# Optimization experiments

Hardware: AMD Instinct MI355X
Metric: run time of the kernel (lower is better)

Reference implementation:

```python
import math
import jax, jax.numpy as jnp
import numpy as np

D_MODEL = 1024
N_HEADS = 16
D_K = D_MODEL // N_HEADS  # 64
D_C = 256
B, S = 2, 2048


def setup_inputs() -> dict:
    key = jax.random.key(0)
    ks = jax.random.split(key, 7)
    sd = lambda fan_in: 1.0 / math.sqrt(fan_in)
    # weights stored as [in, out] so forward is x @ W
    return {
        "x": jax.random.normal(ks[0], (B, S, D_MODEL), dtype=jnp.float32),
        "W_dq": jax.random.uniform(ks[1], (D_MODEL, D_C), minval=-sd(D_MODEL), maxval=sd(D_MODEL), dtype=jnp.float32),
        "W_uq": jax.random.uniform(ks[2], (D_C, N_HEADS * D_K), minval=-sd(D_C), maxval=sd(D_C), dtype=jnp.float32),
        "W_dkv": jax.random.uniform(ks[3], (D_MODEL, D_C), minval=-sd(D_MODEL), maxval=sd(D_MODEL), dtype=jnp.float32),
        "W_uk": jax.random.uniform(ks[4], (D_C, N_HEADS * D_K), minval=-sd(D_C), maxval=sd(D_C), dtype=jnp.float32),
        "W_uv": jax.random.uniform(ks[5], (D_C, N_HEADS * D_K), minval=-sd(D_C), maxval=sd(D_C), dtype=jnp.float32),
        "W_o": jax.random.uniform(ks[6], (N_HEADS * D_K, D_MODEL), minval=-sd(N_HEADS * D_K), maxval=sd(N_HEADS * D_K), dtype=jnp.float32),
    }


def reference(x, W_dq, W_uq, W_dkv, W_uk, W_uv, W_o):
    Bx, Sx, _ = x.shape
    c_q = x @ W_dq                                   # [B,S,d_c]
    Q = (c_q @ W_uq).reshape(Bx, Sx, N_HEADS, D_K)   # [B,S,H,dk]
    c_kv = x @ W_dkv                                 # [B,S,d_c]
    K = (c_kv @ W_uk).reshape(Bx, Sx, N_HEADS, D_K)
    V = (c_kv @ W_uv).reshape(Bx, Sx, N_HEADS, D_K)
    scores = jnp.einsum("bqhd,bkhd->bhqk", Q, K) / math.sqrt(D_K)
    causal = jnp.tril(jnp.ones((Sx, Sx), dtype=bool))
    scores = jnp.where(causal, scores, -jnp.inf)
    attn = jax.nn.softmax(scores, axis=-1)           # [B,H,S,S]
    out = jnp.einsum("bhqk,bkhd->bqhd", attn, V).reshape(Bx, Sx, N_HEADS * D_K)
    return out @ W_o
```

## Files before the change

kernel.cpp:

```cpp
#include <hip/hip_runtime.h>
#include <math.h>

#define AS3 __attribute__((address_space(3)))
#define AS1 __attribute__((address_space(1)))

typedef unsigned short u16;
typedef unsigned int u32;
typedef __bf16 bf16_t;
typedef bf16_t bf16x8 __attribute__((ext_vector_type(8)));
typedef float f32x4 __attribute__((ext_vector_type(4)));
typedef float f32x16 __attribute__((ext_vector_type(16)));
typedef unsigned short u16x4 __attribute__((ext_vector_type(4)));
typedef unsigned short u16x8 __attribute__((ext_vector_type(8)));
typedef unsigned int u32x4 __attribute__((ext_vector_type(4)));

#define NH 16
#define DK 64
#define DC 256
#define DM 1024
#define BB 2
#define SS 2048
#define TT (BB*SS)

__device__ __forceinline__ u16 f2bf(float f) {
    unsigned u = __builtin_bit_cast(unsigned, f);
    unsigned r = (u + 0x7FFFu + ((u >> 16) & 1u)) >> 16;
    return (u16)r;
}

__device__ __forceinline__ float bf2f(u16 h) {
    u32 u = ((u32)h) << 16;
    return __builtin_bit_cast(float, u);
}

__device__ __forceinline__ u32 cvtpk_bf16(float a, float b) {
    u32 d;
    asm("v_cvt_pk_bf16_f32 %0, %1, %2" : "=v"(d) : "v"(a), "v"(b));
    return d;
}

__device__ __forceinline__ bf16x8 lds_frag(const char* p) {
    return __builtin_bit_cast(bf16x8, *reinterpret_cast<const u16x8*>(p));
}

__global__ __launch_bounds__(256) void prep(const float* w0, const float* w1, const float* w2,
                                            const float* w3, const float* w4, const float* w5,
                                            u16* d0, u16* d1, u16* d2, u16* d3, u16* d4, u16* d5) {
    __shared__ float t[32][33];
    const int z = blockIdx.z;
    const float* src; u16* dst; int R, C, opitch;
    switch (z) {
        case 0:  src = w0; dst = d0; R = 1024; C = 256;  opitch = 1024; break;
        case 1:  src = w1; dst = d1; R = 1024; C = 256;  opitch = 1024; break;
        case 2:  src = w2; dst = d2; R = 256;  C = 1024; opitch = 256;  break;
        case 3:  src = w3; dst = d3; R = 256;  C = 1024; opitch = 256;  break;
        case 4:  src = w4; dst = d4; R = 256;  C = 1024; opitch = 256;  break;
        default: src = w5; dst = d5; R = 1024; C = 1024; opitch = 1024; break;
    }
    int c0 = blockIdx.x * 32, r0 = blockIdx.y * 32;
    if (c0 >= C || r0 >= R) return;
    int tx = threadIdx.x & 31, ty = threadIdx.x >> 5;
    #pragma unroll
    for (int p = 0; p < 4; ++p)
        t[ty + 8 * p][tx] = src[(r0 + ty + 8 * p) * C + c0 + tx];
    __syncthreads();
    #pragma unroll
    for (int p = 0; p < 4; ++p)
        dst[(c0 + ty + 8 * p) * opitch + r0 + tx] = f2bf(t[tx][ty + 8 * p]);
}

__global__ __launch_bounds__(256) void gemm_dqkv(const float* __restrict__ X,
                                                 const u16* __restrict__ Bt,
                                                 u16* __restrict__ Cc) {
    __shared__ u16 As[2][64 * 32];
    __shared__ u16 Bs[2][64 * 32];
    const int tid = threadIdx.x;
    const int lane = tid & 63;
    const int w = tid >> 6;
    const int wr = w >> 1, wc = w & 1;
    const int bm = blockIdx.y * 64, bn = blockIdx.x * 64;
    const int l15 = lane & 15, l4 = lane >> 4;
    const int arow = tid >> 2, akc = (tid & 3) * 8;
    const int brow = tid >> 2, bkc = (tid & 3) * 8;

    f32x4 acc[2][2] = {};

    for (int k0 = 0; k0 < 1024; k0 += 64) {
        #pragma unroll
        for (int h = 0; h < 2; ++h) {
            const float* xp = X + (size_t)(bm + arow) * 1024 + k0 + h * 32 + akc;
            float4 v0 = *reinterpret_cast<const float4*>(xp);
            float4 v1 = *reinterpret_cast<const float4*>(xp + 4);
            u32x4 o;
            o.x = cvtpk_bf16(v0.x, v0.y);
            o.y = cvtpk_bf16(v0.z, v0.w);
            o.z = cvtpk_bf16(v1.x, v1.y);
            o.w = cvtpk_bf16(v1.z, v1.w);
            *reinterpret_cast<u32x4*>(&As[h][arow * 32 + akc]) = o;
        }
        #pragma unroll
        for (int h = 0; h < 2; ++h) {
            __builtin_amdgcn_global_load_lds(
                (const AS1 void*)(Bt + (size_t)(bn + brow) * 1024 + k0 + h * 32 + bkc),
                (AS3 void*)((AS3 char*)(AS3 void*)&Bs[h][0] + w * 1024), 16, 0, 0);
        }
        __syncthreads();
        #pragma unroll
        for (int h = 0; h < 2; ++h) {
            bf16x8 a[2], b[2];
            #pragma unroll
            for (int m = 0; m < 2; ++m)
                a[m] = __builtin_bit_cast(bf16x8,
                    *reinterpret_cast<const u16x8*>(&As[h][(wr * 32 + m * 16 + l15) * 32 + l4 * 8]));
            #pragma unroll
            for (int n = 0; n < 2; ++n)
                b[n] = __builtin_bit_cast(bf16x8,
                    *reinterpret_cast<const u16x8*>(&Bs[h][(wc * 32 + n * 16 + l15) * 32 + l4 * 8]));
            #pragma unroll
            for (int m = 0; m < 2; ++m)
                #pragma unroll
                for (int n = 0; n < 2; ++n)
                    acc[m][n] = __builtin_amdgcn_mfma_f32_16x16x32_bf16(a[m], b[n], acc[m][n], 0, 0, 0);
        }
        __syncthreads();
    }
    #pragma unroll
    for (int m = 0; m < 2; ++m) {
        int row = bm + wr * 32 + m * 16 + l4 * 4;
        #pragma unroll
        for (int j = 0; j < 4; ++j)
            #pragma unroll
            for (int n = 0; n < 2; ++n) {
                int col = bn + wc * 32 + n * 16 + l15;
                Cc[(size_t)(row + j) * 512 + col] = f2bf(acc[m][n][j]);
            }
    }
}

__global__ __launch_bounds__(256) void gemm_out(const u16* __restrict__ A,
                                                const u16* __restrict__ Bt,
                                                float* __restrict__ C) {
    __shared__ u16 As[2][64 * 32];
    __shared__ u16 Bs[2][128 * 32];
    const int tid = threadIdx.x;
    const int lane = tid & 63;
    const int w = tid >> 6;
    const int wr = w >> 1, wc = w & 1;
    const int bm = blockIdx.y * 64, bn = blockIdx.x * 128;
    const int l15 = lane & 15, l4 = lane >> 4;

    f32x4 acc[2][4] = {};

    for (int k0 = 0; k0 < 1024; k0 += 64) {
        #pragma unroll
        for (int h = 0; h < 2; ++h) {
            {
                int db = tid * 16;
                int row = db >> 6;
                int kc = (db & 63) >> 1;
                __builtin_amdgcn_global_load_lds(
                    (const AS1 void*)(A + (size_t)(bm + row) * 1024 + k0 + h * 32 + kc),
                    (AS3 void*)((AS3 char*)(AS3 void*)&As[h][0] + w * 1024), 16, 0, 0);
            }
            #pragma unroll
            for (int i = 0; i < 2; ++i) {
                int db = i * 4096 + tid * 16;
                int row = db >> 6;
                int kc = (db & 63) >> 1;
                __builtin_amdgcn_global_load_lds(
                    (const AS1 void*)(Bt + (size_t)(bn + row) * 1024 + k0 + h * 32 + kc),
                    (AS3 void*)((AS3 char*)(AS3 void*)&Bs[h][0] + i * 4096 + w * 1024), 16, 0, 0);
            }
        }
        __syncthreads();
        #pragma unroll
        for (int h = 0; h < 2; ++h) {
            bf16x8 a[2], b[4];
            #pragma unroll
            for (int m = 0; m < 2; ++m)
                a[m] = __builtin_bit_cast(bf16x8,
                    *reinterpret_cast<const u16x8*>(&As[h][(wr * 32 + m * 16 + l15) * 32 + l4 * 8]));
            #pragma unroll
            for (int n = 0; n < 4; ++n)
                b[n] = __builtin_bit_cast(bf16x8,
                    *reinterpret_cast<const u16x8*>(&Bs[h][(wc * 64 + n * 16 + l15) * 32 + l4 * 8]));
            #pragma unroll
            for (int m = 0; m < 2; ++m)
                #pragma unroll
                for (int n = 0; n < 4; ++n)
                    acc[m][n] = __builtin_amdgcn_mfma_f32_16x16x32_bf16(a[m], b[n], acc[m][n], 0, 0, 0);
        }
        __syncthreads();
    }
    #pragma unroll
    for (int m = 0; m < 2; ++m) {
        int row = bm + wr * 32 + m * 16 + l4 * 4;
        #pragma unroll
        for (int j = 0; j < 4; ++j)
            #pragma unroll
            for (int n = 0; n < 4; ++n) {
                int col = bn + wc * 64 + n * 16 + l15;
                C[(size_t)(row + j) * 1024 + col] = acc[m][n][j];
            }
    }
}

template <int OUT_MODE>
__device__ __forceinline__ void gemm_body128(const u16* __restrict__ A, int lda,
                                             const u16* __restrict__ Bt, int ldb,
                                             void* __restrict__ C, int ldc, int K,
                                             int bm, int bn, u16* As, u16* Bs) {
    const int tid = threadIdx.x;
    const int lane = tid & 63;
    const int w = tid >> 6;
    const int wr = w >> 1, wc = w & 1;
    const int l15 = lane & 15, l4 = lane >> 4;

    f32x4 acc[4][4] = {};

    for (int k0 = 0; k0 < K; k0 += 32) {
        #pragma unroll
        for (int i = 0; i < 2; ++i) {
            int db = i * 4096 + tid * 16;
            int row = db >> 6;
            int kc = (db & 63) >> 1;
            __builtin_amdgcn_global_load_lds(
                (const AS1 void*)(A + (size_t)(bm + row) * lda + k0 + kc),
                (AS3 void*)((AS3 char*)(AS3 void*)As + i * 4096 + w * 1024), 16, 0, 0);
            __builtin_amdgcn_global_load_lds(
                (const AS1 void*)(Bt + (size_t)(bn + row) * ldb + k0 + kc),
                (AS3 void*)((AS3 char*)(AS3 void*)Bs + i * 4096 + w * 1024), 16, 0, 0);
        }
        __syncthreads();
        bf16x8 a[4], b[4];
        #pragma unroll
        for (int m = 0; m < 4; ++m)
            a[m] = __builtin_bit_cast(bf16x8,
                *reinterpret_cast<const u16x8*>(&As[(wr * 64 + m * 16 + l15) * 32 + l4 * 8]));
        #pragma unroll
        for (int n = 0; n < 4; ++n)
            b[n] = __builtin_bit_cast(bf16x8,
                *reinterpret_cast<const u16x8*>(&Bs[(wc * 64 + n * 16 + l15) * 32 + l4 * 8]));
        #pragma unroll
        for (int m = 0; m < 4; ++m)
            #pragma unroll
            for (int n = 0; n < 4; ++n)
                acc[m][n] = __builtin_amdgcn_mfma_f32_16x16x32_bf16(a[m], b[n], acc[m][n], 0, 0, 0);
        __syncthreads();
    }
    if (OUT_MODE == 2) {
        #pragma unroll
        for (int m = 0; m < 4; ++m) {
            int row = bm + wr * 64 + m * 16 + l4 * 4;
            int vrow_base = (row >> 11) << 10;
            int scol = row & 2047;
            #pragma unroll
            for (int n = 0; n < 4; ++n) {
                int col = bn + wc * 64 + n * 16 + l15;
                u16x4 ov;
                ov[0] = f2bf(acc[m][n][0]); ov[1] = f2bf(acc[m][n][1]);
                ov[2] = f2bf(acc[m][n][2]); ov[3] = f2bf(acc[m][n][3]);
                *reinterpret_cast<u16x4*>((u16*)C + (size_t)(vrow_base + col) * 2048 + scol) = ov;
            }
        }
    } else {
        #pragma unroll
        for (int m = 0; m < 4; ++m) {
            int row = bm + wr * 64 + m * 16 + l4 * 4;
            #pragma unroll
            for (int j = 0; j < 4; ++j)
                #pragma unroll
                for (int n = 0; n < 4; ++n) {
                    int col = bn + wc * 64 + n * 16 + l15;
                    ((u16*)C)[(size_t)(row + j) * ldc + col] = f2bf(acc[m][n][j]);
                }
        }
    }
}

__global__ __launch_bounds__(256) void gemm_qkv(const u16* __restrict__ c_qkv,
                                                const u16* __restrict__ Wuq_t,
                                                const u16* __restrict__ Wukv_t,
                                                u16* __restrict__ Qb, u16* __restrict__ Kb,
                                                u16* __restrict__ Vt) {
    __shared__ u16 As[128 * 32];
    __shared__ u16 Bs[128 * 32];
    const int bx = blockIdx.x;
    if (bx < 8) {
        gemm_body128<1>(c_qkv, 512, Wuq_t, 256, Qb, 1024, 256,
                        blockIdx.y * 128, bx * 128, As, Bs);
    } else if (bx < 16) {
        gemm_body128<1>(c_qkv + 256, 512, Wukv_t, 256, Kb, 1024, 256,
                        blockIdx.y * 128, (bx - 8) * 128, As, Bs);
    } else {
        gemm_body128<2>(c_qkv + 256, 512, Wukv_t + 1024 * 256, 256, Vt, 0, 256,
                        blockIdx.y * 128, (bx - 16) * 128, As, Bs);
    }
}

__global__ __launch_bounds__(256, 4) void attn_mfma6(const u16* __restrict__ Qb,
                                                     const u16* __restrict__ Kb,
                                                     const u16* __restrict__ VtG,
                                                     u16* __restrict__ O) {
    __shared__ char lds[32768];
    const int bid = blockIdx.x;
    const int bq = 31 - (bid >> 5);
    const int bh = bid & 31;
    const int b = bh >> 4, head = bh & 15;
    const int tid = threadIdx.x;
    const int w = tid >> 6;
    const int lane = tid & 63;
    const int l31 = lane & 31, hi = lane >> 5;
    const int r7 = l31 & 7;
    const int pair = w >> 1, sub = w & 1;
    const int q0 = bq * 64;
    const int qg = q0 + sub * 32 + l31;
    const int rounds = (bq >> 1) + 1;
    const float c2 = 0.125f * 1.44269504088896340736f;
    const float THRraw = 44.3614195558f;

    bf16x8 qf[4];
    {
        const u16* qp = Qb + (size_t)(b * SS + qg) * 1024 + head * 64 + hi * 8;
        #pragma unroll
        for (int kc = 0; kc < 4; ++kc)
            qf[kc] = __builtin_bit_cast(bf16x8, *reinterpret_cast<const u16x8*>(qp + kc * 16));
    }

    f32x16 acc0 = {}, acc1 = {};
    float mrow = -3.0e38f, lrow = 0.f;

#define STAGE2(r_) do { \
    _Pragma("unroll") \
    for (int p_ = 0; p_ < 2; ++p_) { \
        int kt_ = 2 * (r_) + p_; \
        if (kt_ <= bq) { \
            int k0_ = kt_ * 64; \
            char* base_ = lds + p_ * 16384; \
            _Pragma("unroll") \
            for (int c_ = 0; c_ < 2; ++c_) { \
                int i_ = tid + 256 * c_; int row_ = i_ >> 3; int sc_ = (i_ & 7) ^ (row_ & 7); \
                __builtin_amdgcn_global_load_lds( \
                    (const AS1 void*)(Kb + (size_t)(b * SS + k0_ + row_) * 1024 + head * 64 + sc_ * 8), \
                    (AS3 void*)((AS3 char*)(AS3 void*)base_ + c_ * 4096 + w * 1024), 16, 0, 0); \
                __builtin_amdgcn_global_load_lds( \
                    (const AS1 void*)(VtG + (size_t)(bh * 64 + row_) * 2048 + k0_ + sc_ * 8), \
                    (AS3 void*)((AS3 char*)(AS3 void*)base_ + 8192 + c_ * 4096 + w * 1024), 16, 0, 0); \
            } \
        } \
    } } while (0)

    for (int r = 0; r < rounds; ++r) {
        STAGE2(r);
        __syncthreads();
        const int kt = 2 * r + pair;
        if (kt <= bq) {
            const char* Kb_ = lds + pair * 16384;
            const char* Vb_ = Kb_ + 8192;
            const int k0 = kt * 64;
            f32x16 s0 = {}, s1 = {};
            __builtin_amdgcn_s_setprio(1);
            #pragma unroll
            for (int kc = 0; kc < 4; ++kc) {
                bf16x8 kf0 = lds_frag(Kb_ + (l31) * 128 + ((2 * kc + hi) ^ r7) * 16);
                bf16x8 kf1 = lds_frag(Kb_ + (32 + l31) * 128 + ((2 * kc + hi) ^ r7) * 16);
                s0 = __builtin_amdgcn_mfma_f32_32x32x16_bf16(kf0, qf[kc], s0, 0, 0, 0);
                s1 = __builtin_amdgcn_mfma_f32_32x32x16_bf16(kf1, qf[kc], s1, 0, 0, 0);
            }
            __builtin_amdgcn_s_setprio(0);
            if (kt == bq) {
                const int lim = qg - k0 - hi * 4;
                #pragma unroll
                for (int r2 = 0; r2 < 16; ++r2) {
                    const int ko = (r2 & 3) + 8 * (r2 >> 2);
                    s0[r2] = (ko > lim) ? -3.0e38f : s0[r2];
                    s1[r2] = (ko + 32 > lim) ? -3.0e38f : s1[r2];
                }
            }
            float a8[8];
            #pragma unroll
            for (int i = 0; i < 8; ++i)
                a8[i] = fmaxf(fmaxf(s0[2 * i], s0[2 * i + 1]), fmaxf(s1[2 * i], s1[2 * i + 1]));
            float tm = fmaxf(fmaxf(fmaxf(a8[0], a8[1]), fmaxf(a8[2], a8[3])),
                             fmaxf(fmaxf(a8[4], a8[5]), fmaxf(a8[6], a8[7])));
            tm = fmaxf(tm, __shfl_xor(tm, 32));
            bool nofix = __all(tm <= mrow + THRraw);
            float scale = 1.f;
            if (!nofix) {
                float mnew = fmaxf(mrow, tm);
                scale = exp2f((mrow - mnew) * c2);
                mrow = mnew;
            }
            float mc = mrow * c2;
            #pragma unroll
            for (int r2 = 0; r2 < 16; ++r2) {
                s0[r2] = exp2f(__builtin_fmaf(s0[r2], c2, -mc));
                s1[r2] = exp2f(__builtin_fmaf(s1[r2], c2, -mc));
            }
            float c8[8];
            #pragma unroll
            for (int i = 0; i < 8; ++i)
                c8[i] = (s0[2 * i] + s0[2 * i + 1]) + (s1[2 * i] + s1[2 * i + 1]);
            float rsum = ((c8[0] + c8[1]) + (c8[2] + c8[3])) + ((c8[4] + c8[5]) + (c8[6] + c8[7]));
            rsum += __shfl_xor(rsum, 32);
            if (nofix) {
                lrow += rsum;
            } else {
                lrow = lrow * scale + rsum;
                #pragma unroll
                for (int r2 = 0; r2 < 16; ++r2) { acc0[r2] *= scale; acc1[r2] *= scale; }
            }
            u32 cg0[4][2], cg1[4][2];
            #pragma unroll
            for (int g = 0; g < 4; ++g) {
                #pragma unroll
                for (int w2 = 0; w2 < 2; ++w2) {
                    cg0[g][w2] = cvtpk_bf16(s0[4 * g + 2 * w2], s0[4 * g + 2 * w2 + 1]);
                    cg1[g][w2] = cvtpk_bf16(s1[4 * g + 2 * w2], s1[4 * g + 2 * w2 + 1]);
                }
            }
            bf16x8 pa[4];
            #pragma unroll
            for (int ks = 0; ks < 4; ++ks) {
                const int g0 = (2 * ks) & 3, g1 = g0 + 1;
                u32 a0, a1, b0, b1;
                if (ks < 2) { a0 = cg0[g0][0]; a1 = cg0[g0][1]; b0 = cg0[g1][0]; b1 = cg0[g1][1]; }
                else        { a0 = cg1[g0][0]; a1 = cg1[g0][1]; b0 = cg1[g1][0]; b1 = cg1[g1][1]; }
                u32 pa0 = (u32)__shfl_xor((int)a0, 32);
                u32 pa1 = (u32)__shfl_xor((int)a1, 32);
                u32 pb0 = (u32)__shfl_xor((int)b0, 32);
                u32 pb1 = (u32)__shfl_xor((int)b1, 32);
                u32x4 f;
                f.x = hi ? pb0 : a0;
                f.y = hi ? pb1 : a1;
                f.z = hi ? b0 : pa0;
                f.w = hi ? b1 : pa1;
                pa[ks] = __builtin_bit_cast(bf16x8, f);
            }
            __builtin_amdgcn_s_setprio(1);
            #pragma unroll
            for (int ks = 0; ks < 4; ++ks) {
                bf16x8 vf0 = lds_frag(Vb_ + (l31) * 128 + ((2 * ks + hi) ^ r7) * 16);
                bf16x8 vf1 = lds_frag(Vb_ + (32 + l31) * 128 + ((2 * ks + hi) ^ r7) * 16);
                acc0 = __builtin_amdgcn_mfma_f32_32x32x16_bf16(vf0, pa[ks], acc0, 0, 0, 0);
                acc1 = __builtin_amdgcn_mfma_f32_32x32x16_bf16(vf1, pa[ks], acc1, 0, 0, 0);
            }
            __builtin_amdgcn_s_setprio(0);
        }
        __syncthreads();
    }
#undef STAGE2

    u16* partb = (u16*)lds;
    float* mls = (float*)(lds + 18432);
    #pragma unroll
    for (int r2 = 0; r2 < 16; r2 += 2) {
        const int d0 = (r2 & 3) + 8 * (r2 >> 2) + 4 * hi;
        *reinterpret_cast<u32*>(&partb[(w * 32 + l31) * 72 + d0]) =
            cvtpk_bf16(acc0[r2], acc0[r2 + 1]);
        *reinterpret_cast<u32*>(&partb[(w * 32 + l31) * 72 + d0 + 32]) =
            cvtpk_bf16(acc1[r2], acc1[r2 + 1]);
    }
    if (hi == 0) {
        mls[(w * 2 + 0) * 32 + l31] = mrow;
        mls[(w * 2 + 1) * 32 + l31] = lrow;
    }
    __syncthreads();

    {
        const int q = tid >> 2, ds0 = (tid & 3) * 16;
        const int s_ = q >> 5, qq = q & 31;
        const int wa_ = s_, wb_ = 2 + s_;
        float ma = mls[(wa_ * 2 + 0) * 32 + qq], la = mls[(wa_ * 2 + 1) * 32 + qq];
        float mb = mls[(wb_ * 2 + 0) * 32 + qq], lb = mls[(wb_ * 2 + 1) * 32 + qq];
        float mt = fmaxf(ma, mb);
        float wa = exp2f((ma - mt) * c2);
        float wb = exp2f((mb - mt) * c2);
        float lt = la * wa + lb * wb;
        float inv = 1.0f / lt;
        u16x8 pa0 = *reinterpret_cast<const u16x8*>(&partb[(wa_ * 32 + qq) * 72 + ds0]);
        u16x8 pa1 = *reinterpret_cast<const u16x8*>(&partb[(wa_ * 32 + qq) * 72 + ds0 + 8]);
        u16x8 pb0 = *reinterpret_cast<const u16x8*>(&partb[(wb_ * 32 + qq) * 72 + ds0]);
        u16x8 pb1 = *reinterpret_cast<const u16x8*>(&partb[(wb_ * 32 + qq) * 72 + ds0 + 8]);
        u16x8 ov0, ov1;
        #pragma unroll
        for (int i = 0; i < 8; ++i) {
            float v0 = bf2f(pa0[i]) * wa + bf2f(pb0[i]) * wb;
            float v1 = bf2f(pa1[i]) * wa + bf2f(pb1[i]) * wb;
            ov0[i] = f2bf(v0 * inv);
            ov1[i] = f2bf(v1 * inv);
        }
        u16* op = O + (size_t)(b * SS + q0 + q) * 1024 + head * 64 + ds0;
        *reinterpret_cast<u16x8*>(op) = ov0;
        *reinterpret_cast<u16x8*>(op + 8) = ov1;
    }
}


extern "C" void kernel_launch(void* const* d_in, const int* in_sizes, int n_in,
                              void* d_out, int out_size, void* d_ws, size_t ws_size,
                              hipStream_t stream) {
    const float* x     = (const float*)d_in[0];
    const float* W_dq  = (const float*)d_in[1];
    const float* W_uq  = (const float*)d_in[2];
    const float* W_dkv = (const float*)d_in[3];
    const float* W_uk  = (const float*)d_in[4];
    const float* W_uv  = (const float*)d_in[5];
    const float* W_o   = (const float*)d_in[6];
    float* out = (float*)d_out;

    char* ws = (char*)d_ws;
    u16* c_qkv   = (u16*)(ws + (8u << 20));
    u16* Qb      = (u16*)(ws + (12u << 20));
    u16* Kb      = (u16*)(ws + (20u << 20));
    u16* Vt      = (u16*)(ws + (36u << 20));
    u16* attno   = (u16*)(ws + (44u << 20));
    u16* Wdqkv_t = (u16*)(ws + (52u << 20));
    u16* Wuq_t   = (u16*)(ws + (53u << 20));
    u16* Wukv_t  = (u16*)(ws + (53u << 20) + (512u << 10));
    u16* Wo_t    = (u16*)(ws + (55u << 20));

    dim3 blk(256);
    prep<<<dim3(32, 32, 6), blk, 0, stream>>>(W_dq, W_dkv, W_uq, W_uk, W_uv, W_o,
        Wdqkv_t, Wdqkv_t + 256 * 1024, Wuq_t, Wukv_t, Wukv_t + 1024 * 256, Wo_t);
    gemm_dqkv<<<dim3(8, 64), blk, 0, stream>>>(x, Wdqkv_t, c_qkv);
    gemm_qkv<<<dim3(24, 32), blk, 0, stream>>>(c_qkv, Wuq_t, Wukv_t, Qb, Kb, Vt);
    attn_mfma6<<<dim3(1024), blk, 0, stream>>>(Qb, Kb, Vt, attno);
    gemm_out<<<dim3(8, 64), blk, 0, stream>>>(attno, Wo_t, out);
}
```

Measured before the change: 103.7 us.

## Overlap weight transposes with down-projection GEMM and widen up-projection K step

```diff
diff --git a/kernel.cpp b/kernel.cpp
--- a/kernel.cpp
+++ b/kernel.cpp
@@ -43,45 +43,60 @@
     return __builtin_bit_cast(bf16x8, *reinterpret_cast<const u16x8*>(p));
 }
 
-__global__ __launch_bounds__(256) void prep(const float* w0, const float* w1, const float* w2,
-                                            const float* w3, const float* w4, const float* w5,
-                                            u16* d0, u16* d1, u16* d2, u16* d3, u16* d4, u16* d5) {
-    __shared__ float t[32][33];
-    const int z = blockIdx.z;
-    const float* src; u16* dst; int R, C, opitch;
-    switch (z) {
-        case 0:  src = w0; dst = d0; R = 1024; C = 256;  opitch = 1024; break;
-        case 1:  src = w1; dst = d1; R = 1024; C = 256;  opitch = 1024; break;
-        case 2:  src = w2; dst = d2; R = 256;  C = 1024; opitch = 256;  break;
-        case 3:  src = w3; dst = d3; R = 256;  C = 1024; opitch = 256;  break;
-        case 4:  src = w4; dst = d4; R = 256;  C = 1024; opitch = 256;  break;
-        default: src = w5; dst = d5; R = 1024; C = 1024; opitch = 1024; break;
-    }
-    int c0 = blockIdx.x * 32, r0 = blockIdx.y * 32;
-    if (c0 >= C || r0 >= R) return;
+__device__ __forceinline__ void tr_tile(const float* src, u16* dst, int C, int opitch,
+                                        int c0, int r0, float* tbuf) {
+    float (*t)[33] = reinterpret_cast<float(*)[33]>(tbuf);
     int tx = threadIdx.x & 31, ty = threadIdx.x >> 5;
     #pragma unroll
     for (int p = 0; p < 4; ++p)
-        t[ty + 8 * p][tx] = src[(r0 + ty + 8 * p) * C + c0 + tx];
+        t[ty + 8 * p][tx] = src[(size_t)(r0 + ty + 8 * p) * C + c0 + tx];
     __syncthreads();
     #pragma unroll
     for (int p = 0; p < 4; ++p)
-        dst[(c0 + ty + 8 * p) * opitch + r0 + tx] = f2bf(t[tx][ty + 8 * p]);
+        dst[(size_t)(c0 + ty + 8 * p) * opitch + r0 + tx] = f2bf(t[tx][ty + 8 * p]);
+}
+
+__global__ __launch_bounds__(256) void prep(const float* w0, const float* w1,
+                                            u16* d0, u16* d1) {
+    __shared__ float t[32][33];
+    const float* src = blockIdx.z ? w1 : w0;
+    u16* dst = blockIdx.z ? d1 : d0;
+    tr_tile(src, dst, 256, 1024, blockIdx.x * 32, blockIdx.y * 32, &t[0][0]);
 }
 
 __global__ __launch_bounds__(256) void gemm_dqkv(const float* __restrict__ X,
                                                  const u16* __restrict__ Bt,
-                                                 u16* __restrict__ Cc) {
+                                                 u16* __restrict__ Cc,
+                                                 const float* W_uq, const float* W_uk,
+                                                 const float* W_uv, const float* W_o,
+                                                 u16* Wuq_t, u16* Wukv_t, u16* Wo_t) {
     __shared__ u16 As[2][64 * 32];
     __shared__ u16 Bs[2][64 * 32];
+    const int bx = blockIdx.x;
+    if (bx >= 8) {
+        int L = (bx - 8) * 64 + blockIdx.y;
+        float* tbuf = (float*)&As[0][0];
+        if (L < 256) {
+            tr_tile(W_uq, Wuq_t, 1024, 256, (L & 31) * 32, (L >> 5) * 32, tbuf);
+        } else if (L < 512) {
+            int L2 = L - 256;
+            tr_tile(W_uk, Wukv_t, 1024, 256, (L2 & 31) * 32, (L2 >> 5) * 32, tbuf);
+        } else if (L < 768) {
+            int L2 = L - 512;
+            tr_tile(W_uv, Wukv_t + 1024 * 256, 1024, 256, (L2 & 31) * 32, (L2 >> 5) * 32, tbuf);
+        } else {
+            int L2 = L - 768;
+            tr_tile(W_o, Wo_t, 1024, 1024, (L2 & 31) * 32, (L2 >> 5) * 32, tbuf);
+        }
+        return;
+    }
     const int tid = threadIdx.x;
     const int lane = tid & 63;
     const int w = tid >> 6;
     const int wr = w >> 1, wc = w & 1;
-    const int bm = blockIdx.y * 64, bn = blockIdx.x * 64;
+    const int bm = blockIdx.y * 64, bn = bx * 64;
     const int l15 = lane & 15, l4 = lane >> 4;
     const int arow = tid >> 2, akc = (tid & 3) * 8;
-    const int brow = tid >> 2, bkc = (tid & 3) * 8;
 
     f32x4 acc[2][2] = {};
 
@@ -101,7 +116,7 @@
         #pragma unroll
         for (int h = 0; h < 2; ++h) {
             __builtin_amdgcn_global_load_lds(
-                (const AS1 void*)(Bt + (size_t)(bn + brow) * 1024 + k0 + h * 32 + bkc),
+                (const AS1 void*)(Bt + (size_t)(bn + arow) * 1024 + k0 + h * 32 + akc),
                 (AS3 void*)((AS3 char*)(AS3 void*)&Bs[h][0] + w * 1024), 16, 0, 0);
         }
         __syncthreads();
@@ -206,10 +221,10 @@
 }
 
 template <int OUT_MODE>
-__device__ __forceinline__ void gemm_body128(const u16* __restrict__ A, int lda,
-                                             const u16* __restrict__ Bt, int ldb,
-                                             void* __restrict__ C, int ldc, int K,
-                                             int bm, int bn, u16* As, u16* Bs) {
+__device__ __forceinline__ void gemm_body128_bk64(const u16* __restrict__ A, int lda,
+                                                  const u16* __restrict__ Bt, int ldb,
+                                                  void* __restrict__ C, int ldc,
+                                                  int bm, int bn, u16* As, u16* Bs) {
     const int tid = threadIdx.x;
     const int lane = tid & 63;
     const int w = tid >> 6;
@@ -218,34 +233,42 @@
 
     f32x4 acc[4][4] = {};
 
-    for (int k0 = 0; k0 < K; k0 += 32) {
-        #pragma unroll
-        for (int i = 0; i < 2; ++i) {
-            int db = i * 4096 + tid * 16;
-            int row = db >> 6;
-            int kc = (db & 63) >> 1;
-            __builtin_amdgcn_global_load_lds(
-                (const AS1 void*)(A + (size_t)(bm + row) * lda + k0 + kc),
-                (AS3 void*)((AS3 char*)(AS3 void*)As + i * 4096 + w * 1024), 16, 0, 0);
-            __builtin_amdgcn_global_load_lds(
-                (const AS1 void*)(Bt + (size_t)(bn + row) * ldb + k0 + kc),
-                (AS3 void*)((AS3 char*)(AS3 void*)Bs + i * 4096 + w * 1024), 16, 0, 0);
-        }
-        __syncthreads();
-        bf16x8 a[4], b[4];
-        #pragma unroll
-        for (int m = 0; m < 4; ++m)
-            a[m] = __builtin_bit_cast(bf16x8,
-                *reinterpret_cast<const u16x8*>(&As[(wr * 64 + m * 16 + l15) * 32 + l4 * 8]));
-        #pragma unroll
-        for (int n = 0; n < 4; ++n)
-            b[n] = __builtin_bit_cast(bf16x8,
-                *reinterpret_cast<const u16x8*>(&Bs[(wc * 64 + n * 16 + l15) * 32 + l4 * 8]));
-        #pragma unroll
-        for (int m = 0; m < 4; ++m)
+    for (int k0 = 0; k0 < 256; k0 += 64) {
+        #pragma unroll
+        for (int h = 0; h < 2; ++h) {
+            #pragma unroll
+            for (int i = 0; i < 2; ++i) {
+                int db = i * 4096 + tid * 16;
+                int row = db >> 6;
+                int kc = (db & 63) >> 1;
+                __builtin_amdgcn_global_load_lds(
+                    (const AS1 void*)(A + (size_t)(bm + row) * lda + k0 + h * 32 + kc),
+                    (AS3 void*)((AS3 char*)(AS3 void*)(As + (size_t)h * 128 * 32) + i * 4096 + w * 1024), 16, 0, 0);
+                __builtin_amdgcn_global_load_lds(
+                    (const AS1 void*)(Bt + (size_t)(bn + row) * ldb + k0 + h * 32 + kc),
+                    (AS3 void*)((AS3 char*)(AS3 void*)(Bs + (size_t)h * 128 * 32) + i * 4096 + w * 1024), 16, 0, 0);
+            }
+        }
+        __syncthreads();
+        #pragma unroll
+        for (int h = 0; h < 2; ++h) {
+            const u16* Ah = As + (size_t)h * 128 * 32;
+            const u16* Bh = Bs + (size_t)h * 128 * 32;
+            bf16x8 a[4], b[4];
+            #pragma unroll
+            for (int m = 0; m < 4; ++m)
+                a[m] = __builtin_bit_cast(bf16x8,
+                    *reinterpret_cast<const u16x8*>(&Ah[(wr * 64 + m * 16 + l15) * 32 + l4 * 8]));
             #pragma unroll
             for (int n = 0; n < 4; ++n)
-                acc[m][n] = __builtin_amdgcn_mfma_f32_16x16x32_bf16(a[m], b[n], acc[m][n], 0, 0, 0);
+                b[n] = __builtin_bit_cast(bf16x8,
+                    *reinterpret_cast<const u16x8*>(&Bh[(wc * 64 + n * 16 + l15) * 32 + l4 * 8]));
+            #pragma unroll
+            for (int m = 0; m < 4; ++m)
+                #pragma unroll
+                for (int n = 0; n < 4; ++n)
+                    acc[m][n] = __builtin_amdgcn_mfma_f32_16x16x32_bf16(a[m], b[n], acc[m][n], 0, 0, 0);
+        }
         __syncthreads();
     }
     if (OUT_MODE == 2) {
@@ -283,18 +306,18 @@
                                                 const u16* __restrict__ Wukv_t,
                                                 u16* __restrict__ Qb, u16* __restrict__ Kb,
                                                 u16* __restrict__ Vt) {
-    __shared__ u16 As[128 * 32];
-    __shared__ u16 Bs[128 * 32];
+    __shared__ u16 As[2 * 128 * 32];
+    __shared__ u16 Bs[2 * 128 * 32];
     const int bx = blockIdx.x;
     if (bx < 8) {
-        gemm_body128<1>(c_qkv, 512, Wuq_t, 256, Qb, 1024, 256,
-                        blockIdx.y * 128, bx * 128, As, Bs);
+        gemm_body128_bk64<1>(c_qkv, 512, Wuq_t, 256, Qb, 1024,
+                             blockIdx.y * 128, bx * 128, As, Bs);
     } else if (bx < 16) {
-        gemm_body128<1>(c_qkv + 256, 512, Wukv_t, 256, Kb, 1024, 256,
-                        blockIdx.y * 128, (bx - 8) * 128, As, Bs);
+        gemm_body128_bk64<1>(c_qkv + 256, 512, Wukv_t, 256, Kb, 1024,
+                             blockIdx.y * 128, (bx - 8) * 128, As, Bs);
     } else {
-        gemm_body128<2>(c_qkv + 256, 512, Wukv_t + 1024 * 256, 256, Vt, 0, 256,
-                        blockIdx.y * 128, (bx - 16) * 128, As, Bs);
+        gemm_body128_bk64<2>(c_qkv + 256, 512, Wukv_t + 1024 * 256, 256, Vt, 0,
+                             blockIdx.y * 128, (bx - 16) * 128, As, Bs);
     }
 }
 
@@ -521,9 +544,10 @@
     u16* Wo_t    = (u16*)(ws + (55u << 20));
 
     dim3 blk(256);
-    prep<<<dim3(32, 32, 6), blk, 0, stream>>>(W_dq, W_dkv, W_uq, W_uk, W_uv, W_o,
-        Wdqkv_t, Wdqkv_t + 256 * 1024, Wuq_t, Wukv_t, Wukv_t + 1024 * 256, Wo_t);
-    gemm_dqkv<<<dim3(8, 64), blk, 0, stream>>>(x, Wdqkv_t, c_qkv);
+    prep<<<dim3(8, 32, 2), blk, 0, stream>>>(W_dq, W_dkv, Wdqkv_t, Wdqkv_t + 256 * 1024);
+    gemm_dqkv<<<dim3(36, 64), blk, 0, stream>>>(x, Wdqkv_t, c_qkv,
+                                                W_uq, W_uk, W_uv, W_o,
+                                                Wuq_t, Wukv_t, Wo_t);
     gemm_qkv<<<dim3(24, 32), blk, 0, stream>>>(c_qkv, Wuq_t, Wukv_t, Qb, Kb, Vt);
     attn_mfma6<<<dim3(1024), blk, 0, stream>>>(Qb, Kb, Vt, attno);
     gemm_out<<<dim3(8, 64), blk, 0, stream>>>(attno, Wo_t, out);
```

Result: slower. 112.6 us (+8.5%).
